# Kernel optimization log

Hardware: AMD Instinct MI355X
Metric: run time of the kernel (lower is better)

## Reference

```python
import jax, jax.numpy as jnp
import numpy as np

TAU = 1.0       # softmax_temp
SOS_IDX = 1
EOS_IDX = 2
MAX_LEN = 20    # total message length incl. SOS/EOS -> 18 decode steps


def setup_inputs() -> dict:
    key = jax.random.key(0)
    ks = jax.random.split(key, 12)
    B, E, H, V, F = 512, 256, 512, 4096, 512
    T = MAX_LEN - 2
    s = lambda k, shape, sc: jax.random.normal(k, shape, jnp.float32) * sc
    return {
        "proto_a": s(ks[0], (B, F), 1.0),
        "proto_b": s(ks[1], (B, F), 1.0),
        "W_init": s(ks[2], (H, 2 * F), (2 * F) ** -0.5),
        "b_init": jnp.zeros((H,), jnp.float32),
        "W_ih": s(ks[3], (3 * H, E), E ** -0.5),
        "W_hh": s(ks[4], (3 * H, H), H ** -0.5),
        "b_ih": jnp.zeros((3 * H,), jnp.float32),
        "b_hh": jnp.zeros((3 * H,), jnp.float32),
        "W_out": s(ks[5], (V, H), H ** -0.5),
        "b_out": jnp.zeros((V,), jnp.float32),
        "emb": s(ks[6], (V, E), 1.0),
        # uniforms in (0,1) turned into Gumbel noise inside reference
        "u_gumbel": jax.random.uniform(ks[7], (T, B, V), jnp.float32, 1e-6, 1.0 - 1e-6),
    }


def reference(proto_a, proto_b, W_init, b_init, W_ih, W_hh, b_ih, b_hh,
              W_out, b_out, emb, u_gumbel):
    B = proto_a.shape[0]
    V = W_out.shape[0]
    # init_h(cat(prototypes, 1)) -> h0 [B, H]
    h0 = jnp.concatenate([proto_a, proto_b], axis=1) @ W_init.T + b_init
    sos = jnp.zeros((B, V), h0.dtype).at[:, SOS_IDX].set(1.0)
    eos = jnp.zeros((B, V), h0.dtype).at[:, EOS_IDX].set(1.0)
    x0 = sos @ emb  # [B, E]
    g = -jnp.log(-jnp.log(u_gumbel))  # Gumbel(0,1) noise, [T, B, V]

    def step(carry, gt):
        h, x = carry  # h [B,H], x [B,E]
        # PyTorch single-step GRU cell
        gi = x @ W_ih.T + b_ih
        gh = h @ W_hh.T + b_hh
        ir, iz, inn = jnp.split(gi, 3, axis=-1)
        hr, hz, hn = jnp.split(gh, 3, axis=-1)
        r = jax.nn.sigmoid(ir + hr)
        z = jax.nn.sigmoid(iz + hz)
        n = jnp.tanh(inn + r * hn)
        h_new = (1.0 - z) * n + z * h
        logits = h_new @ W_out.T + b_out  # [B, V]
        # gumbel_softmax(tau, hard=False) then straight-through hard one-hot
        y = jax.nn.softmax((logits + gt) / TAU, axis=-1)
        hard = jax.nn.one_hot(jnp.argmax(y, axis=-1), V, dtype=y.dtype)
        onehot = hard - jax.lax.stop_gradient(y) + y
        return (h_new, onehot @ emb), onehot

    _, toks = jax.lax.scan(step, (h0, x0), g)  # toks [T, B, V]
    lang = jnp.concatenate([sos[:, None], jnp.swapaxes(toks, 0, 1), eos[:, None]], axis=1)
    return lang  # [B, MAX_LEN, V]
```

## Files before the change

kernel.cpp:

```cpp
#include <hip/hip_runtime.h>
#include <hip/hip_bf16.h>
#include <math.h>

#define B_ 512
#define E_ 256
#define H_ 512
#define V_ 4096
#define T_ 18
#define L_ 20
#define MARGIN_ 0.04f
#define CCAP_ 64

typedef __attribute__((ext_vector_type(8))) short bf16x8;
typedef __attribute__((ext_vector_type(4))) float f32x4;

__global__ __launch_bounds__(256) void kprep32(const float* __restrict__ pa,
                                               const float* __restrict__ pb,
                                               const float* __restrict__ Wout,
                                               float* __restrict__ cat,
                                               __hip_bfloat16* __restrict__ WB) {
  int idx = blockIdx.x * 256 + threadIdx.x;
  if (idx < 524288) {
    int b = idx >> 10, k = idx & 1023;
    cat[idx] = (k < 512) ? pa[b * 512 + k] : pb[b * 512 + (k - 512)];
  } else {
    int i = idx - 524288;
    WB[i] = __float2bfloat16(Wout[i]);
  }
}

__global__ __launch_bounds__(256) void sgemm128(const float* __restrict__ A,
                                                const float* __restrict__ W,
                                                float* __restrict__ P,
                                                int N, int lda, int kPer) {
  __shared__ float As[16][132];
  __shared__ float Bs[16][132];
  const int tid = threadIdx.x;
  const int tx = tid & 15, ty = tid >> 4;
  const int bn = blockIdx.x * 128, bm = blockIdx.y * 128;
  const int k0 = blockIdx.z * kPer;
  const size_t pOff = (size_t)blockIdx.z * (size_t)gridDim.y * 128 * N;
  const int r1 = tid >> 2;
  const int kq = (tid & 3) * 4;

  float acc[8][8] = {};
  for (int kb = 0; kb < kPer; kb += 16) {
    const float* Ap = A + (size_t)(bm + r1) * lda + k0 + kb + kq;
    const float* Wp = W + (size_t)(bn + r1) * lda + k0 + kb + kq;
    float4 a1 = *reinterpret_cast<const float4*>(Ap);
    float4 a2 = *reinterpret_cast<const float4*>(Ap + (size_t)64 * lda);
    float4 b1 = *reinterpret_cast<const float4*>(Wp);
    float4 b2 = *reinterpret_cast<const float4*>(Wp + (size_t)64 * lda);
    As[kq + 0][r1] = a1.x; As[kq + 1][r1] = a1.y;
    As[kq + 2][r1] = a1.z; As[kq + 3][r1] = a1.w;
    As[kq + 0][r1 + 64] = a2.x; As[kq + 1][r1 + 64] = a2.y;
    As[kq + 2][r1 + 64] = a2.z; As[kq + 3][r1 + 64] = a2.w;
    Bs[kq + 0][r1] = b1.x; Bs[kq + 1][r1] = b1.y;
    Bs[kq + 2][r1] = b1.z; Bs[kq + 3][r1] = b1.w;
    Bs[kq + 0][r1 + 64] = b2.x; Bs[kq + 1][r1 + 64] = b2.y;
    Bs[kq + 2][r1 + 64] = b2.z; Bs[kq + 3][r1 + 64] = b2.w;
    __syncthreads();
#pragma unroll
    for (int kk = 0; kk < 16; ++kk) {
      float a[8], b[8];
#pragma unroll
      for (int i = 0; i < 8; ++i) a[i] = As[kk][ty * 8 + i];
#pragma unroll
      for (int j = 0; j < 8; ++j) b[j] = Bs[kk][tx * 8 + j];
#pragma unroll
      for (int i = 0; i < 8; ++i)
#pragma unroll
        for (int j = 0; j < 8; ++j) acc[i][j] = fmaf(a[i], b[j], acc[i][j]);
    }
    __syncthreads();
  }
#pragma unroll
  for (int i = 0; i < 8; ++i) {
    size_t r = (size_t)(bm + ty * 8 + i);
    float4 v0 = make_float4(acc[i][0], acc[i][1], acc[i][2], acc[i][3]);
    float4 v1 = make_float4(acc[i][4], acc[i][5], acc[i][6], acc[i][7]);
    float4* dst = reinterpret_cast<float4*>(P + pOff + r * N + bn + tx * 8);
    dst[0] = v0;
    dst[1] = v1;
  }
}

__global__ __launch_bounds__(256) void reduceH0(const float* __restrict__ parts,
                                                const float* __restrict__ binit,
                                                float* __restrict__ h,
                                                __hip_bfloat16* __restrict__ hB) {
  int i = blockIdx.x * 256 + threadIdx.x;
  double s = (double)binit[i & 511];
#pragma unroll
  for (int c = 0; c < 8; ++c) s += (double)parts[(size_t)c * 262144 + i];
  float f = (float)s;
  h[i] = f;
  hB[i] = __float2bfloat16(f);
}

__device__ __forceinline__ void gh_gemm_body(const float* __restrict__ h,
                                             const float* __restrict__ Whh,
                                             float* __restrict__ ghP,
                                             int gid, int tid, char* smemRaw) {
  float (*As)[132] = reinterpret_cast<float(*)[132]>(smemRaw);
  float (*Bs)[132] = reinterpret_cast<float(*)[132]>(smemRaw + 8448);
  const int tx = tid & 15, ty = tid >> 4;
  const int bx = gid % 12, by = (gid / 12) & 3, bz = gid / 48;
  const int bn = bx * 128, bm = by * 128;
  const int k0 = bz * 64;
  const size_t pOff = (size_t)bz * 786432;
  const int r1 = tid >> 2, kq = (tid & 3) * 4;
  float acc[8][8] = {};
  for (int kb = 0; kb < 64; kb += 16) {
    const float* Ap = h   + (size_t)(bm + r1) * H_ + k0 + kb + kq;
    const float* Wp = Whh + (size_t)(bn + r1) * H_ + k0 + kb + kq;
    float4 a1 = *reinterpret_cast<const float4*>(Ap);
    float4 a2 = *reinterpret_cast<const float4*>(Ap + (size_t)64 * H_);
    float4 b1 = *reinterpret_cast<const float4*>(Wp);
    float4 b2 = *reinterpret_cast<const float4*>(Wp + (size_t)64 * H_);
    As[kq + 0][r1] = a1.x; As[kq + 1][r1] = a1.y;
    As[kq + 2][r1] = a1.z; As[kq + 3][r1] = a1.w;
    As[kq + 0][r1 + 64] = a2.x; As[kq + 1][r1 + 64] = a2.y;
    As[kq + 2][r1 + 64] = a2.z; As[kq + 3][r1 + 64] = a2.w;
    Bs[kq + 0][r1] = b1.x; Bs[kq + 1][r1] = b1.y;
    Bs[kq + 2][r1] = b1.z; Bs[kq + 3][r1] = b1.w;
    Bs[kq + 0][r1 + 64] = b2.x; Bs[kq + 1][r1 + 64] = b2.y;
    Bs[kq + 2][r1 + 64] = b2.z; Bs[kq + 3][r1 + 64] = b2.w;
    __syncthreads();
#pragma unroll
    for (int kk = 0; kk < 16; ++kk) {
      float a[8], b[8];
#pragma unroll
      for (int i = 0; i < 8; ++i) a[i] = As[kk][ty * 8 + i];
#pragma unroll
      for (int j = 0; j < 8; ++j) b[j] = Bs[kk][tx * 8 + j];
#pragma unroll
      for (int i = 0; i < 8; ++i)
#pragma unroll
        for (int j = 0; j < 8; ++j) acc[i][j] = fmaf(a[i], b[j], acc[i][j]);
    }
    __syncthreads();
  }
#pragma unroll
  for (int i = 0; i < 8; ++i) {
    size_t r = (size_t)(bm + ty * 8 + i);
    float4 v0 = make_float4(acc[i][0], acc[i][1], acc[i][2], acc[i][3]);
    float4 v1 = make_float4(acc[i][4], acc[i][5], acc[i][6], acc[i][7]);
    float4* dst = reinterpret_cast<float4*>(ghP + pOff + r * 1536 + bn + tx * 8);
    dst[0] = v0;
    dst[1] = v1;
  }
}

__device__ __forceinline__ void screen_body(const __hip_bfloat16* __restrict__ hB,
                                            const __hip_bfloat16* __restrict__ WoutB,
                                            float* __restrict__ loP,
                                            int bid, int tid) {
  const int wave = tid >> 6, lane = tid & 63;
  const int bx = bid & 63, by = bid >> 6;
  const int bm = by * 64 + wave * 16;
  const int bn = bx * 64;
  const int rA = lane & 15, g = lane >> 4;
  const __hip_bfloat16* ha = hB + (size_t)(bm + rA) * H_ + g * 8;
  const __hip_bfloat16* wb = WoutB + (size_t)(bn + rA) * H_ + g * 8;
  f32x4 acc[4] = {};
  for (int k0 = 0; k0 < H_; k0 += 32) {
    bf16x8 a = *reinterpret_cast<const bf16x8*>(ha + k0);
#pragma unroll
    for (int j = 0; j < 4; ++j) {
      bf16x8 b = *reinterpret_cast<const bf16x8*>(wb + (size_t)j * 16 * H_ + k0);
      acc[j] = __builtin_amdgcn_mfma_f32_16x16x32_bf16(a, b, acc[j], 0, 0, 0);
    }
  }
#pragma unroll
  for (int j = 0; j < 4; ++j)
#pragma unroll
    for (int r = 0; r < 4; ++r)
      loP[(size_t)(bm + g * 4 + r) * V_ + bn + j * 16 + rA] = acc[j][r];
}

__device__ __forceinline__ void gates_body(const float* __restrict__ ghP,
                                           const float* __restrict__ giP,
                                           const float* __restrict__ bih,
                                           const float* __restrict__ bhh,
                                           int tok, float* __restrict__ h,
                                           __hip_bfloat16* __restrict__ hB,
                                           int bid, int tid) {
  const float* g0 = giP + (size_t)tok * 1536;
  size_t base = (size_t)bid * 1536;
#pragma unroll
  for (int c = 0; c < 2; ++c) {
    int j = c * 256 + tid;
    int idx = bid * 512 + j;
    double gr = (double)bhh[j], gz = (double)bhh[512 + j], gn = (double)bhh[1024 + j];
#pragma unroll
    for (int s = 0; s < 8; ++s) {
      const float* p = ghP + (size_t)s * 786432 + base;
      gr += (double)p[j]; gz += (double)p[512 + j]; gn += (double)p[1024 + j];
    }
    float ir  = g0[j]        + bih[j];
    float iz  = g0[512 + j]  + bih[512 + j];
    float inn = g0[1024 + j] + bih[1024 + j];
    float r = 1.f / (1.f + expf(-(ir + (float)gr)));
    float z = 1.f / (1.f + expf(-(iz + (float)gz)));
    float n = tanhf(inn + r * (float)gn);
    float hn = (1.f - z) * n + z * h[idx];
    h[idx] = hn;
    hB[idx] = __float2bfloat16(hn);
  }
}

__device__ __forceinline__ int pick_body(const float* __restrict__ loP,
                                         const float* __restrict__ h,
                                         const float* __restrict__ Wout,
                                         const float* __restrict__ bout,
                                         const float* __restrict__ ub,
                                         int bid, int tid, char* smemRaw) {
  double* sd    = reinterpret_cast<double*>(smemRaw);
  float*  sv    = reinterpret_cast<float*>(smemRaw + 2048);
  int*    si    = reinterpret_cast<int*>(smemRaw + 3072);
  int*    pre   = reinterpret_cast<int*>(smemRaw + 4096);
  int*    candV = reinterpret_cast<int*>(smemRaw + 5120);
  double* bestS = reinterpret_cast<double*>(smemRaw + 5408);
  int*    bestV = reinterpret_cast<int*>(smemRaw + 5416);
  const float* l0 = loP + (size_t)bid * V_;
  float sloc[16];
  float best = -1e30f; int bi = 0x7fffffff;
#pragma unroll
  for (int i = 0; i < 16; ++i) {
    int v = tid + 256 * i;
    float s = l0[v] + bout[v] - logf(-logf(ub[v]));
    sloc[i] = s;
    if (s > best) { best = s; bi = v; }
  }
  sv[tid] = best; si[tid] = bi;
  __syncthreads();
  for (int st = 128; st > 0; st >>= 1) {
    if (tid < st) {
      float ov = sv[tid + st]; int oi = si[tid + st];
      if (ov > sv[tid] || (ov == sv[tid] && oi < si[tid])) { sv[tid] = ov; si[tid] = oi; }
    }
    __syncthreads();
  }
  float smax = sv[0];
  int amax = si[0];
  __syncthreads();
  int c = 0; int lv[16];
#pragma unroll
  for (int i = 0; i < 16; ++i)
    if (sloc[i] >= smax - MARGIN_) { if (c < 16) lv[c] = tid + 256 * i; ++c; }
  pre[tid] = c;
  __syncthreads();
  for (int off = 1; off < 256; off <<= 1) {
    int vv = (tid >= off) ? pre[tid - off] : 0;
    __syncthreads();
    pre[tid] += vv;
    __syncthreads();
  }
  int tot = pre[255];
  int base = pre[tid] - c;
  if (tot <= CCAP_)
    for (int q = 0; q < c; ++q) candV[base + q] = lv[q];
  __syncthreads();
  int tok;
  if (tot == 1) {
    tok = amax;
  } else if (tot <= CCAP_) {
    const float* hb = h + (size_t)bid * H_;
    if (tid == 0) { *bestS = -1e300; *bestV = 0x7fffffff; }
    __syncthreads();
    for (int ci = 0; ci < tot; ++ci) {
      int v = candV[ci];
      const float* wr = Wout + (size_t)v * H_;
      double p = (double)hb[tid] * (double)wr[tid]
               + (double)hb[tid + 256] * (double)wr[tid + 256];
      sd[tid] = p;
      __syncthreads();
      for (int st = 128; st > 0; st >>= 1) {
        if (tid < st) sd[tid] += sd[tid + st];
        __syncthreads();
      }
      if (tid == 0) {
        double s = sd[0] + (double)bout[v] - log(-log((double)ub[v]));
        if (s > *bestS || (s == *bestS && v < *bestV)) { *bestS = s; *bestV = v; }
      }
      __syncthreads();
    }
    tok = *bestV;
  } else {
    const float* hb = h + (size_t)bid * H_;
    double dbest = -1e300; bi = 0x7fffffff;
    for (int i = 0; i < 16; ++i) {
      int v = tid + 256 * i;
      const float* wr = Wout + (size_t)v * H_;
      double dot = 0.0;
      for (int k = 0; k < H_; ++k) dot = fma((double)hb[k], (double)wr[k], dot);
      double s = dot + (double)bout[v] - log(-log((double)ub[v]));
      if (s > dbest) { dbest = s; bi = v; }
    }
    sd[tid] = dbest; si[tid] = bi;
    __syncthreads();
    for (int st = 128; st > 0; st >>= 1) {
      if (tid < st) {
        double ov = sd[tid + st]; int oi = si[tid + st];
        if (ov > sd[tid] || (ov == sd[tid] && oi < si[tid])) { sd[tid] = ov; si[tid] = oi; }
      }
      __syncthreads();
    }
    tok = si[0];
  }
  return tok;
}

__global__ __launch_bounds__(256) void gates_init(const float* __restrict__ ghP,
                                                  const float* __restrict__ giP,
                                                  const float* __restrict__ bih,
                                                  const float* __restrict__ bhh,
                                                  float* __restrict__ h,
                                                  __hip_bfloat16* __restrict__ hB) {
  gates_body(ghP, giP, bih, bhh, 1, h, hB, blockIdx.x, threadIdx.x);
}

__global__ __launch_bounds__(256) void fusedA(const float* __restrict__ h,
                                              const float* __restrict__ Whh,
                                              const __hip_bfloat16* __restrict__ hB,
                                              const __hip_bfloat16* __restrict__ WoutB,
                                              float* __restrict__ ghP,
                                              float* __restrict__ loP,
                                              int doGemm) {
  __shared__ __align__(16) char smemRaw[16896];
  const int bid = blockIdx.x, tid = threadIdx.x;
  if (bid < 512) {
    screen_body(hB, WoutB, loP, bid, tid);
  } else if (doGemm) {
    gh_gemm_body(h, Whh, ghP, bid - 512, tid, smemRaw);
  }
}

__global__ __launch_bounds__(256) void fusedB(const float* __restrict__ loP,
                                              float* __restrict__ h,
                                              const float* __restrict__ Wout,
                                              const float* __restrict__ bout,
                                              const float* __restrict__ u,
                                              const float* __restrict__ ghP,
                                              const float* __restrict__ giP,
                                              const float* __restrict__ bih,
                                              const float* __restrict__ bhh,
                                              __hip_bfloat16* __restrict__ hB,
                                              int* __restrict__ toks,
                                              int t, int doGates) {
  __shared__ __align__(16) char smemRaw[5440];
  const int bid = blockIdx.x, tid = threadIdx.x;
  const float* ub = u + (size_t)bid * V_;
  int tok = pick_body(loP, h, Wout, bout, ub, bid, tid, smemRaw);
  if (tid == 0) toks[t * B_ + bid] = tok;
  __syncthreads();
  if (doGates)
    gates_body(ghP, giP, bih, bhh, tok, h, hB, bid, tid);
}

__global__ __launch_bounds__(256) void kfinal32(float* __restrict__ out,
                                                const int* __restrict__ toks) {
  size_t c = (size_t)blockIdx.x * 256 + threadIdx.x;
  size_t e0 = c * 4;
  int v0 = (int)(e0 & (size_t)(V_ - 1));
  size_t row = e0 >> 12;
  int p = (int)(row % L_);
  int b = (int)(row / L_);
  int tok;
  if (p == 0)           tok = 1;
  else if (p == L_ - 1) tok = 2;
  else                  tok = toks[(p - 1) * B_ + b];
  float4 val = make_float4(0.f, 0.f, 0.f, 0.f);
  int d = tok - v0;
  if (d >= 0 && d < 4) {
    if (d == 0) val.x = 1.f; else if (d == 1) val.y = 1.f;
    else if (d == 2) val.z = 1.f; else val.w = 1.f;
  }
  reinterpret_cast<float4*>(out)[c] = val;
}

__global__ void kmark_ws(float* out) {
  if (threadIdx.x == 0) out[0] = 16.0f;
}
__global__ void kmark_resolver(float* out) {
  if (threadIdx.x == 0) out[2] = 11.0f;
}

extern "C" void kernel_launch(void* const* d_in, const int* in_sizes, int n_in,
                              void* d_out, int out_size, void* d_ws, size_t ws_size,
                              hipStream_t stream) {
  static const int EXPECT[12] = {262144, 262144, 524288, 512, 393216, 786432,
                                 1536, 1536, 2097152, 4096, 1048576, 37748736};
  const float* R[12];
  bool resolved = (n_in == 12);
  if (resolved) {
    bool used[12] = {};
    for (int i = 0; i < 12; ++i) {
      int f = -1;
      for (int j = 0; j < 12; ++j)
        if (!used[j] && in_sizes[j] == EXPECT[i]) { f = j; break; }
      if (f < 0) { resolved = false; break; }
      used[f] = true;
      R[i] = (const float*)d_in[f];
    }
  }
  if (!resolved)
    for (int i = 0; i < 12 && i < n_in; ++i) R[i] = (const float*)d_in[i];

  const float *pa = R[0], *pb = R[1], *Winit = R[2], *binit = R[3],
              *Wih = R[4], *Whh = R[5], *bih = R[6], *bhh = R[7],
              *Wout = R[8], *bout = R[9], *emb = R[10], *ug = R[11];
  float* out = (float*)d_out;

  const size_t TOK_BYTES = (size_t)T_ * B_ * sizeof(int);
  if (ws_size < TOK_BYTES) { kmark_ws<<<1, 64, 0, stream>>>(out); return; }
  int* toks = (int*)d_ws;

  const size_t SC_FLOATS = 16121856;
  float* sc;
  if (ws_size >= 40960 + SC_FLOATS * sizeof(float)) {
    sc = (float*)((char*)d_ws + 40960);
  } else {
    sc = (float*)d_out;
  }
  float* h    = sc;
  float* giP  = sc + 262144;
  float* ghP  = sc + 6553600;
  float* loP  = sc + 12845056;
  __hip_bfloat16* hB    = (__hip_bfloat16*)(sc + 14942208);
  __hip_bfloat16* WoutB = (__hip_bfloat16*)(sc + 15073280);
  float* cat  = ghP;
  float* h0P  = ghP + 524288;

  kprep32<<<10240, 256, 0, stream>>>(pa, pb, Wout, cat, WoutB);
  sgemm128<<<dim3(4, 4, 8), 256, 0, stream>>>(cat, Winit, h0P, 512, 1024, 128);
  reduceH0<<<1024, 256, 0, stream>>>(h0P, binit, h, hB);
  sgemm128<<<dim3(12, 32, 1), 256, 0, stream>>>(emb, Wih, giP, 1536, 256, 256);
  sgemm128<<<dim3(12, 4, 8), 256, 0, stream>>>(h, Whh, ghP, 1536, 512, 64);
  gates_init<<<512, 256, 0, stream>>>(ghP, giP, bih, bhh, h, hB);

  for (int t = 0; t < T_; ++t) {
    const float* uslice = ug + (size_t)t * B_ * V_;
    int notLast = (t < T_ - 1) ? 1 : 0;
    fusedA<<<896, 256, 0, stream>>>(h, Whh, hB, WoutB, ghP, loP, notLast);
    fusedB<<<512, 256, 0, stream>>>(loP, h, Wout, bout, uslice, ghP, giP,
                                    bih, bhh, hB, toks, t, notLast);
  }

  kfinal32<<<40960, 256, 0, stream>>>(out, toks);
  if (!resolved) kmark_resolver<<<1, 64, 0, stream>>>(out);
}
```

Baseline: 1.069 ms.

## Use wave shuffles in pick reductions, prefetch gh partials, reorder fusedA blocks, vectorize prep

Block-wide shared-memory tree reductions in the token pick are replaced with 64-lane shuffle reductions plus a 4-wave combine, and the prefix scan runs only when there are multiple candidates. fusedB now loads and sums the split-K gh partials before the pick so that latency overlaps the pick work. fusedA places its GEMM blocks first so they are scheduled early. The prep kernel is vectorized with float4 loads and stores. These changes cut barriers and serialized latency in the per-step kernels, at the cost of higher register pressure in fusedB.

Measured after the change: 945.5 us. -11.5%, faster.

```diff
diff --git a/kernel.cpp b/kernel.cpp
--- a/kernel.cpp
+++ b/kernel.cpp
@@ -20,12 +20,23 @@
                                                float* __restrict__ cat,
                                                __hip_bfloat16* __restrict__ WB) {
   int idx = blockIdx.x * 256 + threadIdx.x;
-  if (idx < 524288) {
-    int b = idx >> 10, k = idx & 1023;
-    cat[idx] = (k < 512) ? pa[b * 512 + k] : pb[b * 512 + (k - 512)];
+  if (idx < 131072) {
+    int e0 = idx * 4;
+    int b = e0 >> 10, k = e0 & 1023;
+    float4 v = (k < 512) ? *reinterpret_cast<const float4*>(pa + (size_t)b * 512 + k)
+                         : *reinterpret_cast<const float4*>(pb + (size_t)b * 512 + (k - 512));
+    *reinterpret_cast<float4*>(cat + e0) = v;
   } else {
-    int i = idx - 524288;
-    WB[i] = __float2bfloat16(Wout[i]);
+    int e0 = (idx - 131072) * 4;
+    float4 w = *reinterpret_cast<const float4*>(Wout + e0);
+    __hip_bfloat16 b0 = __float2bfloat16(w.x), b1 = __float2bfloat16(w.y);
+    __hip_bfloat16 b2 = __float2bfloat16(w.z), b3 = __float2bfloat16(w.w);
+    ushort4 o;
+    o.x = *reinterpret_cast<unsigned short*>(&b0);
+    o.y = *reinterpret_cast<unsigned short*>(&b1);
+    o.z = *reinterpret_cast<unsigned short*>(&b2);
+    o.w = *reinterpret_cast<unsigned short*>(&b3);
+    *reinterpret_cast<ushort4*>(WB + e0) = o;
   }
 }
 
@@ -217,12 +228,14 @@
                                          const float* __restrict__ ub,
                                          int bid, int tid, char* smemRaw) {
   double* sd    = reinterpret_cast<double*>(smemRaw);
-  float*  sv    = reinterpret_cast<float*>(smemRaw + 2048);
-  int*    si    = reinterpret_cast<int*>(smemRaw + 3072);
-  int*    pre   = reinterpret_cast<int*>(smemRaw + 4096);
-  int*    candV = reinterpret_cast<int*>(smemRaw + 5120);
-  double* bestS = reinterpret_cast<double*>(smemRaw + 5408);
-  int*    bestV = reinterpret_cast<int*>(smemRaw + 5416);
+  int*    pre   = reinterpret_cast<int*>(smemRaw + 2048);
+  int*    candV = reinterpret_cast<int*>(smemRaw + 3072);
+  float*  swv   = reinterpret_cast<float*>(smemRaw + 3328);
+  int*    swi   = reinterpret_cast<int*>(smemRaw + 3344);
+  int*    sct   = reinterpret_cast<int*>(smemRaw + 3360);
+  double* bestS = reinterpret_cast<double*>(smemRaw + 3376);
+  int*    bestV = reinterpret_cast<int*>(smemRaw + 3384);
+  const int lane = tid & 63, wv = tid >> 6;
   const float* l0 = loP + (size_t)bid * V_;
   float sloc[16];
   float best = -1e30f; int bi = 0x7fffffff;
@@ -233,55 +246,64 @@
     sloc[i] = s;
     if (s > best) { best = s; bi = v; }
   }
-  sv[tid] = best; si[tid] = bi;
+#pragma unroll
+  for (int off = 1; off < 64; off <<= 1) {
+    float ov = __shfl_xor(best, off, 64);
+    int   oi = __shfl_xor(bi,  off, 64);
+    if (ov > best || (ov == best && oi < bi)) { best = ov; bi = oi; }
+  }
+  if (lane == 0) { swv[wv] = best; swi[wv] = bi; }
   __syncthreads();
-  for (int st = 128; st > 0; st >>= 1) {
-    if (tid < st) {
-      float ov = sv[tid + st]; int oi = si[tid + st];
-      if (ov > sv[tid] || (ov == sv[tid] && oi < si[tid])) { sv[tid] = ov; si[tid] = oi; }
-    }
-    __syncthreads();
-  }
-  float smax = sv[0];
-  int amax = si[0];
+  float smax = swv[0]; int amax = swi[0];
+#pragma unroll
+  for (int w = 1; w < 4; ++w) {
+    float ov = swv[w]; int oi = swi[w];
+    if (ov > smax || (ov == smax && oi < amax)) { smax = ov; amax = oi; }
+  }
+  int c = 0;
+#pragma unroll
+  for (int i = 0; i < 16; ++i) if (sloc[i] >= smax - MARGIN_) ++c;
+  int csum = c;
+#pragma unroll
+  for (int off = 1; off < 64; off <<= 1) csum += __shfl_xor(csum, off, 64);
+  if (lane == 0) sct[wv] = csum;
   __syncthreads();
-  int c = 0; int lv[16];
-#pragma unroll
-  for (int i = 0; i < 16; ++i)
-    if (sloc[i] >= smax - MARGIN_) { if (c < 16) lv[c] = tid + 256 * i; ++c; }
-  pre[tid] = c;
-  __syncthreads();
-  for (int off = 1; off < 256; off <<= 1) {
-    int vv = (tid >= off) ? pre[tid - off] : 0;
-    __syncthreads();
-    pre[tid] += vv;
-    __syncthreads();
-  }
-  int tot = pre[255];
-  int base = pre[tid] - c;
-  if (tot <= CCAP_)
-    for (int q = 0; q < c; ++q) candV[base + q] = lv[q];
-  __syncthreads();
+  int tot = sct[0] + sct[1] + sct[2] + sct[3];
+
   int tok;
   if (tot == 1) {
     tok = amax;
   } else if (tot <= CCAP_) {
+    int lv[16];
+    int cc = 0;
+#pragma unroll
+    for (int i = 0; i < 16; ++i)
+      if (sloc[i] >= smax - MARGIN_) { if (cc < 16) lv[cc] = tid + 256 * i; ++cc; }
+    pre[tid] = cc;
+    __syncthreads();
+    for (int off = 1; off < 256; off <<= 1) {
+      int vv = (tid >= off) ? pre[tid - off] : 0;
+      __syncthreads();
+      pre[tid] += vv;
+      __syncthreads();
+    }
+    int base = pre[tid] - cc;
+    for (int q = 0; q < cc; ++q) candV[base + q] = lv[q];
+    if (tid == 0) { *bestS = -1e300; *bestV = 0x7fffffff; }
+    __syncthreads();
     const float* hb = h + (size_t)bid * H_;
-    if (tid == 0) { *bestS = -1e300; *bestV = 0x7fffffff; }
-    __syncthreads();
     for (int ci = 0; ci < tot; ++ci) {
       int v = candV[ci];
       const float* wr = Wout + (size_t)v * H_;
       double p = (double)hb[tid] * (double)wr[tid]
                + (double)hb[tid + 256] * (double)wr[tid + 256];
-      sd[tid] = p;
+#pragma unroll
+      for (int off = 1; off < 64; off <<= 1) p += __shfl_xor(p, off, 64);
+      if (lane == 0) sd[wv] = p;
       __syncthreads();
-      for (int st = 128; st > 0; st >>= 1) {
-        if (tid < st) sd[tid] += sd[tid + st];
-        __syncthreads();
-      }
       if (tid == 0) {
-        double s = sd[0] + (double)bout[v] - log(-log((double)ub[v]));
+        double s = sd[0] + sd[1] + sd[2] + sd[3]
+                 + (double)bout[v] - log(-log((double)ub[v]));
         if (s > *bestS || (s == *bestS && v < *bestV)) { *bestS = s; *bestV = v; }
       }
       __syncthreads();
@@ -289,25 +311,29 @@
     tok = *bestV;
   } else {
     const float* hb = h + (size_t)bid * H_;
-    double dbest = -1e300; bi = 0x7fffffff;
+    double dbest = -1e300; int dbi = 0x7fffffff;
     for (int i = 0; i < 16; ++i) {
       int v = tid + 256 * i;
       const float* wr = Wout + (size_t)v * H_;
       double dot = 0.0;
       for (int k = 0; k < H_; ++k) dot = fma((double)hb[k], (double)wr[k], dot);
       double s = dot + (double)bout[v] - log(-log((double)ub[v]));
-      if (s > dbest) { dbest = s; bi = v; }
-    }
-    sd[tid] = dbest; si[tid] = bi;
-    __syncthreads();
-    for (int st = 128; st > 0; st >>= 1) {
-      if (tid < st) {
-        double ov = sd[tid + st]; int oi = si[tid + st];
-        if (ov > sd[tid] || (ov == sd[tid] && oi < si[tid])) { sd[tid] = ov; si[tid] = oi; }
-      }
-      __syncthreads();
-    }
-    tok = si[0];
+      if (s > dbest) { dbest = s; dbi = v; }
+    }
+#pragma unroll
+    for (int off = 1; off < 64; off <<= 1) {
+      double od = __shfl_xor(dbest, off, 64);
+      int    oi = __shfl_xor(dbi,  off, 64);
+      if (od > dbest || (od == dbest && oi < dbi)) { dbest = od; dbi = oi; }
+    }
+    if (lane == 0) { sd[wv] = dbest; pre[wv] = dbi; }
+    __syncthreads();
+    double bs = sd[0]; int bv = pre[0];
+#pragma unroll
+    for (int w = 1; w < 4; ++w) {
+      if (sd[w] > bs || (sd[w] == bs && pre[w] < bv)) { bs = sd[w]; bv = pre[w]; }
+    }
+    tok = bv;
   }
   return tok;
 }
@@ -330,10 +356,10 @@
                                               int doGemm) {
   __shared__ __align__(16) char smemRaw[16896];
   const int bid = blockIdx.x, tid = threadIdx.x;
-  if (bid < 512) {
-    screen_body(hB, WoutB, loP, bid, tid);
-  } else if (doGemm) {
-    gh_gemm_body(h, Whh, ghP, bid - 512, tid, smemRaw);
+  if (bid < 384) {
+    if (doGemm) gh_gemm_body(h, Whh, ghP, bid, tid, smemRaw);
+  } else {
+    screen_body(hB, WoutB, loP, bid - 384, tid);
   }
 }
 
@@ -351,12 +377,48 @@
                                               int t, int doGates) {
   __shared__ __align__(16) char smemRaw[5440];
   const int bid = blockIdx.x, tid = threadIdx.x;
+  const int j0 = tid, j1 = 256 + tid;
+  double gr0 = (double)bhh[j0], gz0 = (double)bhh[512 + j0], gn0 = (double)bhh[1024 + j0];
+  double gr1 = (double)bhh[j1], gz1 = (double)bhh[512 + j1], gn1 = (double)bhh[1024 + j1];
+  if (doGates) {
+    size_t base = (size_t)bid * 1536;
+#pragma unroll
+    for (int s = 0; s < 8; ++s) {
+      const float* p = ghP + (size_t)s * 786432 + base;
+      gr0 += (double)p[j0]; gz0 += (double)p[512 + j0]; gn0 += (double)p[1024 + j0];
+      gr1 += (double)p[j1]; gz1 += (double)p[512 + j1]; gn1 += (double)p[1024 + j1];
+    }
+  }
   const float* ub = u + (size_t)bid * V_;
   int tok = pick_body(loP, h, Wout, bout, ub, bid, tid, smemRaw);
   if (tid == 0) toks[t * B_ + bid] = tok;
-  __syncthreads();
-  if (doGates)
-    gates_body(ghP, giP, bih, bhh, tok, h, hB, bid, tid);
+  if (doGates) {
+    const float* g0 = giP + (size_t)tok * 1536;
+    {
+      int idx = bid * 512 + j0;
+      float ir  = g0[j0]        + bih[j0];
+      float iz  = g0[512 + j0]  + bih[512 + j0];
+      float inn = g0[1024 + j0] + bih[1024 + j0];
+      float r = 1.f / (1.f + expf(-(ir + (float)gr0)));
+      float z = 1.f / (1.f + expf(-(iz + (float)gz0)));
+      float n = tanhf(inn + r * (float)gn0);
+      float hn = (1.f - z) * n + z * h[idx];
+      h[idx] = hn;
+      hB[idx] = __float2bfloat16(hn);
+    }
+    {
+      int idx = bid * 512 + j1;
+      float ir  = g0[j1]        + bih[j1];
+      float iz  = g0[512 + j1]  + bih[512 + j1];
+      float inn = g0[1024 + j1] + bih[1024 + j1];
+      float r = 1.f / (1.f + expf(-(ir + (float)gr1)));
+      float z = 1.f / (1.f + expf(-(iz + (float)gz1)));
+      float n = tanhf(inn + r * (float)gn1);
+      float hn = (1.f - z) * n + z * h[idx];
+      h[idx] = hn;
+      hB[idx] = __float2bfloat16(hn);
+    }
+  }
 }
 
 __global__ __launch_bounds__(256) void kfinal32(float* __restrict__ out,
@@ -433,7 +495,7 @@
   float* cat  = ghP;
   float* h0P  = ghP + 524288;
 
-  kprep32<<<10240, 256, 0, stream>>>(pa, pb, Wout, cat, WoutB);
+  kprep32<<<2560, 256, 0, stream>>>(pa, pb, Wout, cat, WoutB);
   sgemm128<<<dim3(4, 4, 8), 256, 0, stream>>>(cat, Winit, h0P, 512, 1024, 128);
   reduceH0<<<1024, 256, 0, stream>>>(h0P, binit, h, hB);
   sgemm128<<<dim3(12, 32, 1), 256, 0, stream>>>(emb, Wih, giP, 1536, 256, 256);
```
